# Optimization experiments

Measured on AMD Instinct MI355X. Metric: run time of the kernel, lower is better.

The kernel has to match this reference:

```python
import jax, jax.numpy as jnp
import numpy as np

B_SZ, SEQ, D_MODEL = 2, 4096, 2048
EXPAND, D_STATE, D_CONV = 2, 16, 4
D_INNER = EXPAND * D_MODEL          # 4096
DT_RANK = -(-D_MODEL // 16)         # 128


def setup_inputs() -> dict:
    key = jax.random.key(0)
    ks = jax.random.split(key, 9)
    s = 0.02
    hidden_states = jax.random.normal(ks[0], (B_SZ, SEQ, D_MODEL), jnp.float32)
    W_in = jax.random.normal(ks[1], (2 * D_INNER, D_MODEL), jnp.float32) * s
    conv_w = jax.random.normal(ks[2], (D_INNER, D_CONV), jnp.float32) * 0.2
    conv_b = jnp.zeros((D_INNER,), jnp.float32)
    W_x = jax.random.normal(ks[3], (DT_RANK + 2 * D_STATE, D_INNER), jnp.float32) * s
    W_dt = jax.random.normal(ks[4], (D_INNER, DT_RANK), jnp.float32) * (DT_RANK ** -0.5)
    # dt bias so softplus(dt) ~ [1e-3, 0.1] as in Mamba init
    u = jax.random.uniform(ks[5], (D_INNER,), jnp.float32)
    dt = jnp.exp(u * (np.log(0.1) - np.log(1e-3)) + np.log(1e-3))
    dt_bias = dt + jnp.log(-jnp.expm1(-dt))  # inverse softplus
    # S4D-real init: A = -[1..d_state] per channel (kept negative for stability)
    A = -jnp.tile(jnp.arange(1.0, D_STATE + 1.0, dtype=jnp.float32), (D_INNER, 1))
    D = jnp.ones((D_INNER,), jnp.float32)
    W_out = jax.random.normal(ks[6], (D_MODEL, D_INNER), jnp.float32) * s
    return {"hidden_states": hidden_states, "W_in": W_in, "conv_w": conv_w,
            "conv_b": conv_b, "W_x": W_x, "W_dt": W_dt, "dt_bias": dt_bias,
            "A": A, "D": D, "W_out": W_out}


def _mamba_fwd(hidden_states, W_in, conv_w, conv_b, W_x, W_dt, dt_bias, A, D, W_out):
    # in_proj -> (B, L, 2*d_inner); split into x and gate z
    xz = jnp.einsum('bld,ed->ble', hidden_states, W_in)
    x, z = jnp.split(xz, 2, axis=-1)                    # (B,L,d_inner) each
    # causal depthwise conv1d over L (kernel d_conv), then SiLU
    d_conv = conv_w.shape[1]
    xp = jnp.pad(x, ((0, 0), (d_conv - 1, 0), (0, 0)))
    L = x.shape[1]
    xc = conv_b
    acc = jnp.zeros_like(x)
    for k in range(d_conv):                             # small fixed loop (4 taps)
        acc = acc + xp[:, k:k + L, :] * conv_w[:, k]
    x = jax.nn.silu(acc + conv_b)
    # x_proj -> dt_rank + 2*d_state
    ssm = jnp.einsum('bld,ed->ble', x, W_x)
    dt_r, Bm, Cm = jnp.split(ssm, [DT_RANK, DT_RANK + D_STATE], axis=-1)
    delta = jax.nn.softplus(jnp.einsum('blr,dr->bld', dt_r, W_dt) + dt_bias)
    # selective scan: h_t = exp(delta_t*A) h_{t-1} + delta_t*B_t*u_t ; y_t = C_t.h_t
    def step(state, inp):
        d_t, u_t, B_t, C_t = inp                        # (B,Di),(B,Di),(B,N),(B,N)
        dA = jnp.exp(d_t[..., None] * A)                # (B,Di,N)
        state = state * dA + (d_t * u_t)[..., None] * B_t[:, None, :]
        y = jnp.einsum('bdn,bn->bd', state, C_t)
        return state, y
    init = jnp.zeros((x.shape[0], D_INNER, D_STATE), jnp.float32)
    xs = (jnp.swapaxes(delta, 0, 1), jnp.swapaxes(x, 0, 1),
          jnp.swapaxes(Bm, 0, 1), jnp.swapaxes(Cm, 0, 1))
    _, ys = jax.lax.scan(step, init, xs)
    y = jnp.swapaxes(ys, 0, 1) + x * D                  # D skip connection
    y = y * jax.nn.silu(z)                              # gate
    return jnp.einsum('bld,md->blm', y, W_out)


def reference(hidden_states, W_in, conv_w, conv_b, W_x, W_dt, dt_bias, A, D, W_out):
    return _mamba_fwd(hidden_states, W_in, conv_w, conv_b, W_x, W_dt,
                      dt_bias, A, D, W_out)
```

## Files before the change

### kernel.cpp

```cpp
#include <hip/hip_runtime.h>
#include <hip/hip_bf16.h>
#include <cstdint>
#include <cstddef>

typedef _Float16 f16x8 __attribute__((ext_vector_type(8)));
typedef _Float16 f16x4 __attribute__((ext_vector_type(4)));
typedef float    f32x4 __attribute__((ext_vector_type(4)));

#define AS1 __attribute__((address_space(1)))
#define AS3 __attribute__((address_space(3)))

static constexpr int B_SZ = 2, SEQ = 4096, D_MODEL = 2048;
static constexpr int D_INNER = 4096, D_STATE = 16, D_CONV = 4, DT_RANK = 128;
static constexpr int M_ROWS = B_SZ * SEQ;
static constexpr int SSM_W  = DT_RANK + 2 * D_STATE;

__global__ __launch_bounds__(256) void k_cvt_all(
    const float* __restrict__ s0, const float* __restrict__ s1,
    const float* __restrict__ s2, const float* __restrict__ s3,
    const float* __restrict__ s4,
    _Float16* __restrict__ d0, _Float16* __restrict__ d1,
    _Float16* __restrict__ d2, _Float16* __restrict__ d3,
    _Float16* __restrict__ d4) {
    const int i = blockIdx.x * 256 + threadIdx.x;
    const float* s; _Float16* d; int off;
    if (i < 4194304)      { s = s0; d = d0; off = i; }
    else if (i < 8388608) { s = s1; d = d1; off = i - 4194304; }
    else if (i < 8552448) { s = s2; d = d2; off = i - 8388608; }
    else if (i < 8683520) { s = s3; d = d3; off = i - 8552448; }
    else                  { s = s4; d = d4; off = i - 8683520; }
    f32x4 v = ((const f32x4*)s)[off];
    f16x4 h;
    h[0] = (_Float16)v[0]; h[1] = (_Float16)v[1];
    h[2] = (_Float16)v[2]; h[3] = (_Float16)v[3];
    ((f16x4*)d)[off] = h;
}

template <int EPI>
__global__ __launch_bounds__(512, 2) void k_gemm256p(
    const _Float16* __restrict__ A, const _Float16* __restrict__ Bm, int K, int nby,
    void* __restrict__ out0, void* __restrict__ out1, int ldc) {
    __shared__ _Float16 lA[2][256][64];
    __shared__ _Float16 lB[2][256][64];
    constexpr int LBUF  = 32768;
    constexpr int LBUFH = 16384;

    const int tid = threadIdx.x, l = tid & 63, w = tid >> 6;
    const int fr = l & 15, fq = l >> 4;
    const int wrA = (w >> 2) * 128;
    const int wcB = (w & 3) * 64;

    const int nwg = gridDim.x, qq = nwg >> 3;
    const int id = (blockIdx.x & 7) * qq + (blockIdx.x >> 3);
    const int by = id % nby, bx = id / nby;
    const int tileM = by * 256, tileN = bx * 256;

    const int rsub = l >> 3;
    const int gco  = ((l & 7) ^ rsub) << 3;
    const int swz0 = (fq ^ (fr & 7)) << 4;

    const char* cA = (const char*)lA;
    const char* cB = (const char*)lB;
    const int bA0 = (wrA + fr) * 128 + swz0;
    const int bA1 = bA0 ^ 64;
    const int bB0 = (wcB + fr) * 128 + swz0;
    const int bB1 = bB0 ^ 64;

    const _Float16* pA[4];
    const _Float16* pB[4];
    _Float16* dA[4];
    _Float16* dB[4];
#pragma unroll
    for (int u = 0; u < 4; ++u) {
        const int brow = (u >> 1) * 128 + (w * 2 + (u & 1)) * 8;
        pA[u] = A  + (size_t)(tileM + brow + rsub) * K + gco;
        pB[u] = Bm + (size_t)(tileN + brow + rsub) * K + gco;
        dA[u] = &lA[0][brow][0];
        dB[u] = &lB[0][brow][0];
    }

    const int NK = K >> 6;

    f32x4 acc[8][4];
#pragma unroll
    for (int m = 0; m < 8; m++)
#pragma unroll
        for (int n = 0; n < 4; n++) acc[m][n] = (f32x4)0.f;

#pragma unroll
    for (int t = 0; t < 2; ++t) {
#pragma unroll
        for (int u = 0; u < 4; ++u)
            __builtin_amdgcn_global_load_lds((const AS1 void*)(pA[u] + t * 64),
                (AS3 void*)(dA[u] + t * LBUFH), 16, 0, 0);
#pragma unroll
        for (int u = 0; u < 4; ++u)
            __builtin_amdgcn_global_load_lds((const AS1 void*)(pB[u] + t * 64),
                (AS3 void*)(dB[u] + t * LBUFH), 16, 0, 0);
    }
#pragma unroll
    for (int u = 0; u < 4; ++u) { pA[u] += 128; pB[u] += 128; }
    asm volatile("s_waitcnt vmcnt(8)" ::: "memory");
    __builtin_amdgcn_s_barrier();

    f16x8 af[4][2], bf0[2][2], bf1[2][2];

#define MFMA_QUAD(MO, NO, BF)                                                        \
    __builtin_amdgcn_s_setprio(1);                                                   \
    _Pragma("unroll") for (int m = 0; m < 4; ++m)                                    \
    _Pragma("unroll") for (int n = 0; n < 2; ++n)                                    \
    _Pragma("unroll") for (int kk = 0; kk < 2; ++kk)                                 \
        acc[(MO) + m][(NO) + n] = __builtin_amdgcn_mfma_f32_16x16x32_f16(            \
            af[m][kk], BF[n][kk], acc[(MO) + m][(NO) + n], 0, 0, 0);                 \
    __builtin_amdgcn_s_setprio(0);

#define KTILE(BUF, KOFF, PF, DOEND)                                                  \
          \
    _Pragma("unroll")                                                                \
    for (int m = 0; m < 4; ++m) {                                                    \
        af[m][0] = *(const f16x8*)(cA + (BUF) * LBUF + bA0 + m * 2048);              \
        af[m][1] = *(const f16x8*)(cA + (BUF) * LBUF + bA1 + m * 2048);              \
    }                                                                                \
    _Pragma("unroll")                                                                \
    for (int n = 0; n < 2; ++n) {                                                    \
        bf0[n][0] = *(const f16x8*)(cB + (BUF) * LBUF + bB0 + n * 2048);             \
        bf0[n][1] = *(const f16x8*)(cB + (BUF) * LBUF + bB1 + n * 2048);             \
    }                                                                                \
    _Pragma("unroll")                                                                \
    for (int n = 0; n < 2; ++n) {                                                    \
        bf1[n][0] = *(const f16x8*)(cB + (BUF) * LBUF + bB0 + (n + 2) * 2048);       \
        bf1[n][1] = *(const f16x8*)(cB + (BUF) * LBUF + bB1 + (n + 2) * 2048);       \
    }                                                                                \
    asm volatile("s_waitcnt lgkmcnt(4)" ::: "memory");     \
    __builtin_amdgcn_sched_barrier(0);                                               \
    MFMA_QUAD(0, 0, bf0)                                                             \
    asm volatile("s_waitcnt lgkmcnt(0)" ::: "memory");                 \
    __builtin_amdgcn_sched_barrier(0);                                               \
    MFMA_QUAD(0, 2, bf1)                                                             \
    __builtin_amdgcn_s_barrier();                \
    _Pragma("unroll")                                                                \
    for (int m = 0; m < 4; ++m) {                                                    \
        af[m][0] = *(const f16x8*)(cA + (BUF) * LBUF + bA0 + (m + 4) * 2048);        \
        af[m][1] = *(const f16x8*)(cA + (BUF) * LBUF + bA1 + (m + 4) * 2048);        \
    }                                                                                \
    if (PF) {                                                                        \
        _Pragma("unroll")                                                            \
        for (int u = 0; u < 4; ++u)                                                  \
            __builtin_amdgcn_global_load_lds((const AS1 void*)(pB[u] + (KOFF)),      \
                (AS3 void*)(dB[u] + (BUF) * LBUFH), 16, 0, 0);                       \
    }                                                                                \
    asm volatile("s_waitcnt lgkmcnt(0)" ::: "memory");               \
    __builtin_amdgcn_sched_barrier(0);                                               \
    MFMA_QUAD(4, 0, bf0)                                                             \
    __builtin_amdgcn_s_barrier();               \
    if (PF) {                                                                        \
        _Pragma("unroll")                                                            \
        for (int u = 0; u < 4; ++u)                                                  \
            __builtin_amdgcn_global_load_lds((const AS1 void*)(pA[u] + (KOFF)),      \
                (AS3 void*)(dA[u] + (BUF) * LBUFH), 16, 0, 0);                       \
    }                                                                                \
    MFMA_QUAD(4, 2, bf1)                                                             \
    if (DOEND) {                                                                     \
        if (PF) { asm volatile("s_waitcnt vmcnt(8)" ::: "memory"); }                 \
        else    { asm volatile("s_waitcnt vmcnt(0)" ::: "memory"); }                 \
        __builtin_amdgcn_s_barrier();                 \
    }

    for (int kt = 0; kt < NK; kt += 2) {
        const bool pf0 = (kt + 2 < NK);
        const bool pf1 = (kt + 3 < NK);
        KTILE(0, 0, pf0, true)
        KTILE(1, 64, pf1, pf0)
#pragma unroll
        for (int u = 0; u < 4; ++u) { pA[u] += 128; pB[u] += 128; }
    }
#undef KTILE
#undef MFMA_QUAD

#pragma unroll
    for (int m = 0; m < 8; ++m) {
#pragma unroll
        for (int n = 0; n < 4; ++n) {
            const int r0 = tileM + wrA + m * 16 + fq * 4;
            const int c  = tileN + wcB + n * 16 + fr;
#pragma unroll
            for (int q = 0; q < 4; ++q) {
                const float  v  = acc[m][n][q];
                const size_t mm = (size_t)(r0 + q);
                if (EPI == 0) {
                    if (c < D_INNER)
                        ((_Float16*)out0)[mm * D_INNER + c] = (_Float16)v;
                    else
                        ((_Float16*)out1)[mm * D_INNER + (c - D_INNER)] = (_Float16)v;
                } else {
                    ((float*)out0)[mm * ldc + c] = v;
                }
            }
        }
    }
}

template <int BM, int BN, int EPI>
__global__ __launch_bounds__(256) void k_gemm_nt(
    const _Float16* __restrict__ A, const _Float16* __restrict__ Bm, int K,
    int lda, int ldb, void* __restrict__ out0, void* __restrict__ out1,
    const float* __restrict__ bias, int ldc) {
    __shared__ _Float16 a_lds[BM][32];
    __shared__ _Float16 b_lds[BN][32];
    constexpr int MR = BM / 32;
    constexpr int NR = BN / 32;
    const int tid  = threadIdx.x;
    const int lane = tid & 63;
    const int wid  = tid >> 6;
    const int wr = wid >> 1, wc = wid & 1;
    const int tileM = blockIdx.y * BM;
    const int tileN = blockIdx.x * BN;

    f32x4 acc[MR][NR];
    for (int i = 0; i < MR; i++)
        for (int j = 0; j < NR; j++) acc[i][j] = (f32x4)0.f;

    constexpr int IS_A = BM / 16;
    constexpr int IS_B = BN / 16;
    const int srow = lane >> 2;
    const int skof = (lane & 3) * 8;
    const int fr = lane & 15, fq = lane >> 4;

    for (int kk = 0; kk < K; kk += 32) {
        if (kk) __syncthreads();
        for (int is = wid; is < IS_A + IS_B; is += 4) {
            const bool isA = is < IS_A;
            const int  li  = isA ? is : is - IS_A;
            const int  row = li * 16 + srow;
            const _Float16* g =
                isA ? (A  + (size_t)(tileM + row) * lda + kk + skof)
                    : (Bm + (size_t)(tileN + row) * ldb + kk + skof);
            char* lp = ((char*)(isA ? &a_lds[0][0] : &b_lds[0][0])) + (size_t)li * 1024;
            __builtin_amdgcn_global_load_lds((const AS1 void*)g, (AS3 void*)lp, 16, 0, 0);
        }
        __syncthreads();

        f16x8 af[MR], bf[NR];
#pragma unroll
        for (int i = 0; i < MR; i++)
            af[i] = *(const f16x8*)&a_lds[wr * (BM / 2) + i * 16 + fr][fq * 8];
#pragma unroll
        for (int j = 0; j < NR; j++)
            bf[j] = *(const f16x8*)&b_lds[wc * (BN / 2) + j * 16 + fr][fq * 8];
#pragma unroll
        for (int i = 0; i < MR; i++)
#pragma unroll
            for (int j = 0; j < NR; j++)
                acc[i][j] = __builtin_amdgcn_mfma_f32_16x16x32_f16(af[i], bf[j], acc[i][j], 0, 0, 0);
    }

#pragma unroll
    for (int i = 0; i < MR; i++) {
#pragma unroll
        for (int j = 0; j < NR; j++) {
            const int r0 = tileM + wr * (BM / 2) + i * 16 + fq * 4;
            const int c  = tileN + wc * (BN / 2) + j * 16 + fr;
#pragma unroll
            for (int q = 0; q < 4; q++) {
                const float  v = acc[i][j][q];
                const size_t m = (size_t)(r0 + q);
                if (EPI == 1) {
                    ((float*)out0)[m * ldc + c] = v;
                } else if (EPI == 2) {
                    float x  = v + bias[c];
                    float sp = (x > 20.f) ? x : log1pf(__expf(x));
                    ((_Float16*)out0)[m * ldc + c] = (_Float16)sp;
                } else {
                    ((float*)out0)[m * ldc + c] = v;
                    if (c < DT_RANK)
                        ((_Float16*)out1)[m * DT_RANK + c] = (_Float16)v;
                }
            }
        }
    }
}

__global__ __launch_bounds__(256) void k_conv_silu(const _Float16* __restrict__ x,
                                                   const float* __restrict__ w,
                                                   const float* __restrict__ bias,
                                                   _Float16* __restrict__ out) {
    const int idx = blockIdx.x * 256 + threadIdx.x;
    const int d4 = idx & (D_INNER / 4 - 1);
    const int t  = (idx >> 10) & (SEQ - 1);
    const int b  = idx >> 22;
    const int d  = d4 * 4;
    const size_t rowbase = (size_t)b * SEQ * D_INNER;

    f32x4 wv[4];
#pragma unroll
    for (int i = 0; i < 4; i++) wv[i] = ((const f32x4*)w)[d + i];

    float acc[4];
#pragma unroll
    for (int i = 0; i < 4; i++) acc[i] = bias[d + i];
#pragma unroll
    for (int k = 0; k < D_CONV; k++) {
        int ti = t - (D_CONV - 1) + k;
        if (ti < 0) continue;
        f16x4 xv = *(const f16x4*)&x[rowbase + (size_t)ti * D_INNER + d];
#pragma unroll
        for (int i = 0; i < 4; i++) acc[i] += (float)xv[i] * wv[i][k];
    }
    f16x4 o;
#pragma unroll
    for (int i = 0; i < 4; i++) {
        float v = acc[i];
        o[i] = (_Float16)(v / (1.f + __expf(-v)));
    }
    *(f16x4*)&out[rowbase + (size_t)t * D_INNER + d] = o;
}

template <int CH, typename ST>
__global__ __launch_bounds__(256) void k_scan_p1(const _Float16* __restrict__ delta_h,
                                                 const _Float16* __restrict__ xc,
                                                 const float* __restrict__ ssm,
                                                 const float* __restrict__ Aptr,
                                                 ST* __restrict__ Sbuf,
                                                 ST* __restrict__ Pbuf) {
    constexpr int NCH = SEQ / CH;
    constexpr float L2E = 1.44269504088896f;
    const int bid   = blockIdx.x;
    const int dg    = bid & 15;
    const int chunk = (bid >> 4) % NCH;
    const int b     = bid / (16 * NCH);
    const int d     = dg * 256 + threadIdx.x;

    __shared__ float bsh[CH][D_STATE];
    const size_t rb = (size_t)b * SEQ + (size_t)chunk * CH;
    for (int i = threadIdx.x; i < CH * D_STATE; i += 256) {
        int t = i >> 4, n = i & 15;
        bsh[t][n] = ssm[(rb + t) * SSM_W + DT_RANK + n];
    }
    __syncthreads();

    float a2[D_STATE];
#pragma unroll
    for (int n = 0; n < D_STATE; n++) a2[n] = Aptr[(size_t)d * D_STATE + n] * L2E;
    float st[D_STATE];
#pragma unroll
    for (int n = 0; n < D_STATE; n++) st[n] = 0.f;
    float dtsum = 0.f;

    for (int t = 0; t < CH; ++t) {
        const size_t idx = (rb + t) * D_INNER + d;
        const float dt = (float)delta_h[idx];
        const float u  = (float)xc[idx];
        const float du = dt * u;
        dtsum += dt;
#pragma unroll
        for (int n = 0; n < D_STATE; n++) {
            float p = exp2f(dt * a2[n]);
            st[n] = st[n] * p + du * bsh[t][n];
        }
    }
    const size_t ob = ((size_t)(b * NCH + chunk) * D_STATE) * D_INNER + d;
#pragma unroll
    for (int n = 0; n < D_STATE; n++) {
        Sbuf[ob + (size_t)n * D_INNER] = (ST)st[n];
        Pbuf[ob + (size_t)n * D_INNER] = (ST)exp2f(dtsum * a2[n]);
    }
}

template <int NCH, typename ST>
__global__ __launch_bounds__(256) void k_scan_p2(ST* __restrict__ Sbuf,
                                                 const ST* __restrict__ Pbuf) {
    const int id = blockIdx.x * 256 + threadIdx.x;
    const int d = id & (D_INNER - 1);
    const int n = (id >> 12) & 15;
    const int b = id >> 16;
    float h = 0.f;
    for (int c = 0; c < NCH; ++c) {
        const size_t off = ((size_t)((b * NCH + c) * D_STATE + n)) * D_INNER + d;
        const float Pv = (float)Pbuf[off];
        const float Sv = (float)Sbuf[off];
        Sbuf[off] = (ST)h;
        h = Pv * h + Sv;
    }
}

template <int CH, typename ST>
__global__ __launch_bounds__(256) void k_scan_p3(const _Float16* __restrict__ delta_h,
                                                 const _Float16* __restrict__ xc,
                                                 const float* __restrict__ ssm,
                                                 const _Float16* __restrict__ z,
                                                 const float* __restrict__ Aptr,
                                                 const float* __restrict__ Dptr,
                                                 const ST* __restrict__ Sbuf,
                                                 _Float16* __restrict__ y_out) {
    constexpr int NCH = SEQ / CH;
    constexpr float L2E = 1.44269504088896f;
    const int bid   = blockIdx.x;
    const int dg    = bid & 15;
    const int chunk = (bid >> 4) % NCH;
    const int b     = bid / (16 * NCH);
    const int d     = dg * 256 + threadIdx.x;

    __shared__ float bsh[CH][2 * D_STATE];
    const size_t rb = (size_t)b * SEQ + (size_t)chunk * CH;
    for (int i = threadIdx.x; i < CH * 2 * D_STATE; i += 256) {
        int t = i >> 5, j = i & 31;
        bsh[t][j] = ssm[(rb + t) * SSM_W + DT_RANK + j];
    }
    __syncthreads();

    float a2[D_STATE];
#pragma unroll
    for (int n = 0; n < D_STATE; n++) a2[n] = Aptr[(size_t)d * D_STATE + n] * L2E;
    const float Dd = Dptr[d];

    const size_t ob = ((size_t)(b * NCH + chunk) * D_STATE) * D_INNER + d;
    float st[D_STATE];
#pragma unroll
    for (int n = 0; n < D_STATE; n++) st[n] = (float)Sbuf[ob + (size_t)n * D_INNER];

    for (int t = 0; t < CH; ++t) {
        const size_t idx = (rb + t) * D_INNER + d;
        const float dt = (float)delta_h[idx];
        const float u  = (float)xc[idx];
        const float du = dt * u;
        float y = 0.f;
#pragma unroll
        for (int n = 0; n < D_STATE; n++) {
            float p = exp2f(dt * a2[n]);
            st[n] = st[n] * p + du * bsh[t][n];
            y += st[n] * bsh[t][D_STATE + n];
        }
        const float zv = (float)z[idx];
        const float g  = zv / (1.f + __expf(-zv));
        y_out[idx] = (_Float16)((y + u * Dd) * g);
    }
}

__global__ __launch_bounds__(256) void k_scan(const _Float16* __restrict__ delta_h,
                                              const _Float16* __restrict__ xc,
                                              const float* __restrict__ ssm,
                                              const _Float16* __restrict__ z,
                                              const float* __restrict__ Aptr,
                                              const float* __restrict__ Dptr,
                                              _Float16* __restrict__ y_out) {
    const int b = blockIdx.x >> 4;
    const int d = (blockIdx.x & 15) * 256 + threadIdx.x;
    constexpr float L2E = 1.44269504088896f;
    float a2[D_STATE];
#pragma unroll
    for (int n = 0; n < D_STATE; n++) a2[n] = Aptr[(size_t)d * D_STATE + n] * L2E;
    const float Dd = Dptr[d];
    float st[D_STATE];
#pragma unroll
    for (int n = 0; n < D_STATE; n++) st[n] = 0.f;
    __shared__ float bc[128][32];
    const size_t rb = (size_t)b * SEQ;
    for (int tc = 0; tc < SEQ; tc += 128) {
        __syncthreads();
        for (int i = threadIdx.x; i < 128 * 32; i += 256) {
            int tl = i >> 5, j = i & 31;
            bc[tl][j] = ssm[(rb + tc + tl) * SSM_W + DT_RANK + j];
        }
        __syncthreads();
        for (int tl = 0; tl < 128; ++tl) {
            const size_t idx = (rb + tc + tl) * D_INNER + d;
            const float dt = (float)delta_h[idx];
            const float u  = (float)xc[idx];
            const float du = dt * u;
            float y = 0.f;
#pragma unroll
            for (int n = 0; n < D_STATE; n++) {
                float dA = exp2f(dt * a2[n]);
                st[n] = st[n] * dA + du * bc[tl][n];
                y += st[n] * bc[tl][D_STATE + n];
            }
            const float zv = (float)z[idx];
            const float g  = zv / (1.f + __expf(-zv));
            y_out[idx] = (_Float16)((y + u * Dd) * g);
        }
    }
}

template <int CH, typename ST>
static void launch_chunked_scan(const _Float16* delta_h, const _Float16* xc,
                                const float* ssm, const _Float16* z,
                                const float* Aptr, const float* Dptr,
                                ST* S, ST* P, _Float16* y, hipStream_t stream) {
    constexpr int NCH = SEQ / CH;
    k_scan_p1<CH, ST><<<B_SZ * NCH * 16, 256, 0, stream>>>(delta_h, xc, ssm, Aptr, S, P);
    k_scan_p2<NCH, ST><<<(B_SZ * 16 * D_INNER) / 256, 256, 0, stream>>>(S, P);
    k_scan_p3<CH, ST><<<B_SZ * NCH * 16, 256, 0, stream>>>(delta_h, xc, ssm, z, Aptr, Dptr, S, y);
}

extern "C" void kernel_launch(void* const* d_in, const int* in_sizes, int n_in,
                              void* d_out, int out_size, void* d_ws, size_t ws_size,
                              hipStream_t stream) {
    const float* hs    = (const float*)d_in[0];
    const float* W_in  = (const float*)d_in[1];
    const float* convw = (const float*)d_in[2];
    const float* convb = (const float*)d_in[3];
    const float* W_x   = (const float*)d_in[4];
    const float* W_dt  = (const float*)d_in[5];
    const float* dtb   = (const float*)d_in[6];
    const float* Aptr  = (const float*)d_in[7];
    const float* Dptr  = (const float*)d_in[8];
    const float* W_out = (const float*)d_in[9];

    char* ws = (char*)d_ws;
    _Float16* hs_h    = (_Float16*)(ws + 0);
    _Float16* Win_h   = (_Float16*)(ws + 33554432);
    _Float16* y_h     = (_Float16*)(ws + 0);
    _Float16* xraw    = (_Float16*)(ws + 67108864);
    _Float16* delta_h = (_Float16*)(ws + 67108864);
    _Float16* xc      = (_Float16*)(ws + 134217728);
    float*    ssm     = (float*)   (ws + 201326592);
    _Float16* dtr     = (_Float16*)(ws + 206569472);
    _Float16* Wx_h    = (_Float16*)(ws + 208666624);
    _Float16* Wdt_h   = (_Float16*)(ws + 209977344);
    _Float16* Wout_h  = (_Float16*)(ws + 211025920);
    _Float16* z_h     = (_Float16*)d_out;
    const size_t spbase = 227803136ull;

    k_cvt_all<<<42112, 256, 0, stream>>>(hs, W_in, W_x, W_dt, W_out,
                                         hs_h, Win_h, Wx_h, Wdt_h, Wout_h);

    k_gemm256p<0><<<(M_ROWS / 256) * (2 * D_INNER / 256), 512, 0, stream>>>(
        hs_h, Win_h, D_MODEL, M_ROWS / 256, xraw, z_h, 0);

    k_conv_silu<<<(B_SZ * SEQ * (D_INNER / 4)) / 256, 256, 0, stream>>>(xraw, convw, convb, xc);

    k_gemm_nt<128, 32, 3><<<dim3(SSM_W / 32, M_ROWS / 128), 256, 0, stream>>>(
        xc, Wx_h, D_INNER, D_INNER, D_INNER, ssm, dtr, nullptr, SSM_W);

    k_gemm_nt<128, 128, 2><<<dim3(D_INNER / 128, M_ROWS / 128), 256, 0, stream>>>(
        dtr, Wdt_h, DT_RANK, DT_RANK, DT_RANK, delta_h, nullptr, dtb, D_INNER);

    {
        const size_t e64  = (size_t)B_SZ * (SEQ / 64)  * D_STATE * D_INNER;
        const size_t e128 = (size_t)B_SZ * (SEQ / 128) * D_STATE * D_INNER;
        if (ws_size >= spbase + 2 * e64 * sizeof(float)) {
            float* S = (float*)(ws + spbase);
            float* P = S + e64;
            launch_chunked_scan<64, float>(delta_h, xc, ssm, z_h, Aptr, Dptr, S, P, y_h, stream);
        } else if (ws_size >= spbase + 2 * e128 * sizeof(float)) {
            float* S = (float*)(ws + spbase);
            float* P = S + e128;
            launch_chunked_scan<128, float>(delta_h, xc, ssm, z_h, Aptr, Dptr, S, P, y_h, stream);
        } else if (ws_size >= spbase + 2 * e128 * sizeof(_Float16)) {
            _Float16* S = (_Float16*)(ws + spbase);
            _Float16* P = S + e128;
            launch_chunked_scan<128, _Float16>(delta_h, xc, ssm, z_h, Aptr, Dptr, S, P, y_h, stream);
        } else {
            k_scan<<<B_SZ * (D_INNER / 256), 256, 0, stream>>>(delta_h, xc, ssm, z_h, Aptr, Dptr, y_h);
        }
    }

    k_gemm256p<1><<<(M_ROWS / 256) * (D_MODEL / 256), 512, 0, stream>>>(
        y_h, Wout_h, D_INNER, M_ROWS / 256, d_out, nullptr, D_MODEL);
}
```

Baseline: 1.119 ms.

## Fuse dt projection and softplus into chunked scan kernels; restructure big GEMM pipeline

Removes the separate dt_proj GEMM that wrote the full delta tensor to global memory. Both scan passes now recompute delta for their chunk with MFMA from dtr and W_dt, apply bias and softplus, and keep it in LDS. This avoids writing and twice re-reading a large fp16 delta tensor, at the cost of doing the small rank-128 GEMM twice and using more LDS per block. The 256x256 GEMM main loop is also reorganised into k-halves: A fragments for the next tile are preloaded, and A and B are both staged right after a single barrier, replacing the interleaved quadrant schedule.

Result: slower. 2.530 ms (+126.2%).

```diff
diff --git a/kernel.cpp b/kernel.cpp
--- a/kernel.cpp
+++ b/kernel.cpp
@@ -42,8 +42,7 @@
     void* __restrict__ out0, void* __restrict__ out1, int ldc) {
     __shared__ _Float16 lA[2][256][64];
     __shared__ _Float16 lB[2][256][64];
-    constexpr int LBUF  = 32768;
-    constexpr int LBUFH = 16384;
+    constexpr int LBUF = 32768;
 
     const int tid = threadIdx.x, l = tid & 63, w = tid >> 6;
     const int fr = l & 15, fq = l >> 4;
@@ -66,18 +65,9 @@
     const int bB0 = (wcB + fr) * 128 + swz0;
     const int bB1 = bB0 ^ 64;
 
-    const _Float16* pA[4];
-    const _Float16* pB[4];
-    _Float16* dA[4];
-    _Float16* dB[4];
-#pragma unroll
-    for (int u = 0; u < 4; ++u) {
-        const int brow = (u >> 1) * 128 + (w * 2 + (u & 1)) * 8;
-        pA[u] = A  + (size_t)(tileM + brow + rsub) * K + gco;
-        pB[u] = Bm + (size_t)(tileN + brow + rsub) * K + gco;
-        dA[u] = &lA[0][brow][0];
-        dB[u] = &lB[0][brow][0];
-    }
+    const _Float16* Abase = A  + (size_t)tileM * K;
+    const _Float16* Bbase = Bm + (size_t)tileN * K;
+    const int laneOff = rsub * K + gco;
 
     const int NK = K >> 6;
 
@@ -87,95 +77,82 @@
 #pragma unroll
         for (int n = 0; n < 4; n++) acc[m][n] = (f32x4)0.f;
 
-#pragma unroll
-    for (int t = 0; t < 2; ++t) {
-#pragma unroll
-        for (int u = 0; u < 4; ++u)
-            __builtin_amdgcn_global_load_lds((const AS1 void*)(pA[u] + t * 64),
-                (AS3 void*)(dA[u] + t * LBUFH), 16, 0, 0);
-#pragma unroll
-        for (int u = 0; u < 4; ++u)
-            __builtin_amdgcn_global_load_lds((const AS1 void*)(pB[u] + t * 64),
-                (AS3 void*)(dB[u] + t * LBUFH), 16, 0, 0);
-    }
-#pragma unroll
-    for (int u = 0; u < 4; ++u) { pA[u] += 128; pB[u] += 128; }
+#define STAGE_AB(KT2)                                                                 \
+    {                                                                                 \
+        const size_t ko = (size_t)(KT2) * 64;                                         \
+        const int bsel = (KT2) & 1;                                                   \
+        _Pragma("unroll")                                                             \
+        for (int u = 0; u < 4; ++u) {                                                 \
+            const int brow = (u >> 1) * 128 + (w * 2 + (u & 1)) * 8;                  \
+            __builtin_amdgcn_global_load_lds(                                         \
+                (const AS1 void*)(Abase + (size_t)brow * K + ko + laneOff),           \
+                (AS3 void*)&lA[bsel][brow][0], 16, 0, 0);                             \
+        }                                                                             \
+        _Pragma("unroll")                                                             \
+        for (int u = 0; u < 4; ++u) {                                                 \
+            const int brow = (u >> 1) * 128 + (w * 2 + (u & 1)) * 8;                  \
+            __builtin_amdgcn_global_load_lds(                                         \
+                (const AS1 void*)(Bbase + (size_t)brow * K + ko + laneOff),           \
+                (AS3 void*)&lB[bsel][brow][0], 16, 0, 0);                             \
+        }                                                                             \
+    }
+
+    STAGE_AB(0)
+    STAGE_AB(1)
     asm volatile("s_waitcnt vmcnt(8)" ::: "memory");
     __builtin_amdgcn_s_barrier();
 
-    f16x8 af[4][2], bf0[2][2], bf1[2][2];
-
-#define MFMA_QUAD(MO, NO, BF)                                                        \
-    __builtin_amdgcn_s_setprio(1);                                                   \
-    _Pragma("unroll") for (int m = 0; m < 4; ++m)                                    \
-    _Pragma("unroll") for (int n = 0; n < 2; ++n)                                    \
-    _Pragma("unroll") for (int kk = 0; kk < 2; ++kk)                                 \
-        acc[(MO) + m][(NO) + n] = __builtin_amdgcn_mfma_f32_16x16x32_f16(            \
-            af[m][kk], BF[n][kk], acc[(MO) + m][(NO) + n], 0, 0, 0);                 \
+    f16x8 afk0[8], afk1[8], bfk0[4], bfk1[4];
+#pragma unroll
+    for (int m = 0; m < 8; ++m)
+        afk0[m] = *(const f16x8*)(cA + bA0 + m * 2048);
+
+#define MFMA_HALF(AF, BF)                                                             \
+    __builtin_amdgcn_s_setprio(1);                                                    \
+    _Pragma("unroll") for (int m = 0; m < 8; ++m)                                     \
+    _Pragma("unroll") for (int n = 0; n < 4; ++n)                                     \
+        acc[m][n] = __builtin_amdgcn_mfma_f32_16x16x32_f16(                           \
+            AF[m], BF[n], acc[m][n], 0, 0, 0);                                        \
     __builtin_amdgcn_s_setprio(0);
 
-#define KTILE(BUF, KOFF, PF, DOEND)                                                  \
-          \
-    _Pragma("unroll")                                                                \
-    for (int m = 0; m < 4; ++m) {                                                    \
-        af[m][0] = *(const f16x8*)(cA + (BUF) * LBUF + bA0 + m * 2048);              \
-        af[m][1] = *(const f16x8*)(cA + (BUF) * LBUF + bA1 + m * 2048);              \
-    }                                                                                \
-    _Pragma("unroll")                                                                \
-    for (int n = 0; n < 2; ++n) {                                                    \
-        bf0[n][0] = *(const f16x8*)(cB + (BUF) * LBUF + bB0 + n * 2048);             \
-        bf0[n][1] = *(const f16x8*)(cB + (BUF) * LBUF + bB1 + n * 2048);             \
-    }                                                                                \
-    _Pragma("unroll")                                                                \
-    for (int n = 0; n < 2; ++n) {                                                    \
-        bf1[n][0] = *(const f16x8*)(cB + (BUF) * LBUF + bB0 + (n + 2) * 2048);       \
-        bf1[n][1] = *(const f16x8*)(cB + (BUF) * LBUF + bB1 + (n + 2) * 2048);       \
-    }                                                                                \
-    asm volatile("s_waitcnt lgkmcnt(4)" ::: "memory");     \
-    __builtin_amdgcn_sched_barrier(0);                                               \
-    MFMA_QUAD(0, 0, bf0)                                                             \
-    asm volatile("s_waitcnt lgkmcnt(0)" ::: "memory");                 \
-    __builtin_amdgcn_sched_barrier(0);                                               \
-    MFMA_QUAD(0, 2, bf1)                                                             \
-    __builtin_amdgcn_s_barrier();                \
-    _Pragma("unroll")                                                                \
-    for (int m = 0; m < 4; ++m) {                                                    \
-        af[m][0] = *(const f16x8*)(cA + (BUF) * LBUF + bA0 + (m + 4) * 2048);        \
-        af[m][1] = *(const f16x8*)(cA + (BUF) * LBUF + bA1 + (m + 4) * 2048);        \
-    }                                                                                \
-    if (PF) {                                                                        \
-        _Pragma("unroll")                                                            \
-        for (int u = 0; u < 4; ++u)                                                  \
-            __builtin_amdgcn_global_load_lds((const AS1 void*)(pB[u] + (KOFF)),      \
-                (AS3 void*)(dB[u] + (BUF) * LBUFH), 16, 0, 0);                       \
-    }                                                                                \
-    asm volatile("s_waitcnt lgkmcnt(0)" ::: "memory");               \
-    __builtin_amdgcn_sched_barrier(0);                                               \
-    MFMA_QUAD(4, 0, bf0)                                                             \
-    __builtin_amdgcn_s_barrier();               \
-    if (PF) {                                                                        \
-        _Pragma("unroll")                                                            \
-        for (int u = 0; u < 4; ++u)                                                  \
-            __builtin_amdgcn_global_load_lds((const AS1 void*)(pA[u] + (KOFF)),      \
-                (AS3 void*)(dA[u] + (BUF) * LBUFH), 16, 0, 0);                       \
-    }                                                                                \
-    MFMA_QUAD(4, 2, bf1)                                                             \
-    if (DOEND) {                                                                     \
-        if (PF) { asm volatile("s_waitcnt vmcnt(8)" ::: "memory"); }                 \
-        else    { asm volatile("s_waitcnt vmcnt(0)" ::: "memory"); }                 \
-        __builtin_amdgcn_s_barrier();                 \
-    }
+#define KTILE(BUF, NBUF, PF, HN, KT2)                                                 \
+                                      \
+    _Pragma("unroll")                                                                 \
+    for (int n = 0; n < 4; ++n)                                                       \
+        bfk0[n] = *(const f16x8*)(cB + (BUF) * LBUF + bB0 + n * 2048);                \
+    _Pragma("unroll")                                                                 \
+    for (int m = 0; m < 8; ++m)                                                       \
+        afk1[m] = *(const f16x8*)(cA + (BUF) * LBUF + bA1 + m * 2048);                \
+    _Pragma("unroll")                                                                 \
+    for (int n = 0; n < 4; ++n)                                                       \
+        bfk1[n] = *(const f16x8*)(cB + (BUF) * LBUF + bB1 + n * 2048);                \
+    asm volatile("s_waitcnt lgkmcnt(12)" ::: "memory");          \
+    __builtin_amdgcn_sched_barrier(0);                                                \
+    MFMA_HALF(afk0, bfk0)                                                             \
+    asm volatile("s_waitcnt lgkmcnt(0)" ::: "memory");     \
+    __builtin_amdgcn_sched_barrier(0);                                                \
+    __builtin_amdgcn_s_barrier();                              \
+    if (PF) STAGE_AB(KT2)                                                             \
+    if (HN) {                                                                         \
+        if (PF) { asm volatile("s_waitcnt vmcnt(8)" ::: "memory"); }                  \
+        else    { asm volatile("s_waitcnt vmcnt(0)" ::: "memory"); }                  \
+        __builtin_amdgcn_s_barrier();                          \
+        _Pragma("unroll")                                                             \
+        for (int m = 0; m < 8; ++m)                                                   \
+            afk0[m] = *(const f16x8*)(cA + (NBUF) * LBUF + bA0 + m * 2048);           \
+    }                                                                                 \
+    __builtin_amdgcn_sched_barrier(0);                                                \
+    MFMA_HALF(afk1, bfk1)
 
     for (int kt = 0; kt < NK; kt += 2) {
         const bool pf0 = (kt + 2 < NK);
         const bool pf1 = (kt + 3 < NK);
-        KTILE(0, 0, pf0, true)
-        KTILE(1, 64, pf1, pf0)
-#pragma unroll
-        for (int u = 0; u < 4; ++u) { pA[u] += 128; pB[u] += 128; }
+        KTILE(0, 1, pf0, true, kt + 2)
+        KTILE(1, 0, pf1, pf0, kt + 3)
     }
 #undef KTILE
-#undef MFMA_QUAD
+#undef MFMA_HALF
+#undef STAGE_AB
 
 #pragma unroll
     for (int m = 0; m < 8; ++m) {
@@ -316,28 +293,71 @@
 }
 
 template <int CH, typename ST>
-__global__ __launch_bounds__(256) void k_scan_p1(const _Float16* __restrict__ delta_h,
+__global__ __launch_bounds__(256) void k_scan_p1(const _Float16* __restrict__ dtr,
+                                                 const _Float16* __restrict__ Wdt,
+                                                 const float* __restrict__ dtb,
                                                  const _Float16* __restrict__ xc,
                                                  const float* __restrict__ ssm,
                                                  const float* __restrict__ Aptr,
                                                  ST* __restrict__ Sbuf,
                                                  ST* __restrict__ Pbuf) {
     constexpr int NCH = SEQ / CH;
+    constexpr int MR  = CH / 16;
     constexpr float L2E = 1.44269504088896f;
     const int bid   = blockIdx.x;
     const int dg    = bid & 15;
     const int chunk = (bid >> 4) % NCH;
     const int b     = bid / (16 * NCH);
-    const int d     = dg * 256 + threadIdx.x;
-
-    __shared__ float bsh[CH][D_STATE];
+    const int tid   = threadIdx.x;
+    const int lane  = tid & 63, wid = tid >> 6;
+    const int fr = lane & 15, fq = lane >> 4;
     const size_t rb = (size_t)b * SEQ + (size_t)chunk * CH;
-    for (int i = threadIdx.x; i < CH * D_STATE; i += 256) {
+
+    __shared__ float    bsh[CH][D_STATE];
+    __shared__ _Float16 dsh[CH][256];
+
+    {
+        f32x4 acc[MR][4];
+#pragma unroll
+        for (int i = 0; i < MR; ++i)
+#pragma unroll
+            for (int j = 0; j < 4; ++j) acc[i][j] = (f32x4)0.f;
+        const int nbase = wid * 64;
+        for (int kk = 0; kk < DT_RANK; kk += 32) {
+            f16x8 af[MR], bf[4];
+#pragma unroll
+            for (int i = 0; i < MR; ++i)
+                af[i] = *(const f16x8*)&dtr[(rb + i * 16 + fr) * DT_RANK + kk + fq * 8];
+#pragma unroll
+            for (int j = 0; j < 4; ++j)
+                bf[j] = *(const f16x8*)&Wdt[(size_t)(dg * 256 + nbase + j * 16 + fr) * DT_RANK + kk + fq * 8];
+#pragma unroll
+            for (int i = 0; i < MR; ++i)
+#pragma unroll
+                for (int j = 0; j < 4; ++j)
+                    acc[i][j] = __builtin_amdgcn_mfma_f32_16x16x32_f16(af[i], bf[j], acc[i][j], 0, 0, 0);
+        }
+#pragma unroll
+        for (int j = 0; j < 4; ++j) {
+            const int c  = nbase + j * 16 + fr;
+            const float bv = dtb[dg * 256 + c];
+#pragma unroll
+            for (int i = 0; i < MR; ++i)
+#pragma unroll
+                for (int q = 0; q < 4; ++q) {
+                    float x  = acc[i][j][q] + bv;
+                    float sp = (x > 20.f) ? x : log1pf(__expf(x));
+                    dsh[i * 16 + fq * 4 + q][c] = (_Float16)sp;
+                }
+        }
+    }
+    for (int i = tid; i < CH * D_STATE; i += 256) {
         int t = i >> 4, n = i & 15;
         bsh[t][n] = ssm[(rb + t) * SSM_W + DT_RANK + n];
     }
     __syncthreads();
 
+    const int d = dg * 256 + tid;
     float a2[D_STATE];
 #pragma unroll
     for (int n = 0; n < D_STATE; n++) a2[n] = Aptr[(size_t)d * D_STATE + n] * L2E;
@@ -347,9 +367,8 @@
     float dtsum = 0.f;
 
     for (int t = 0; t < CH; ++t) {
-        const size_t idx = (rb + t) * D_INNER + d;
-        const float dt = (float)delta_h[idx];
-        const float u  = (float)xc[idx];
+        const float dt = (float)dsh[t][tid];
+        const float u  = (float)xc[(rb + t) * D_INNER + d];
         const float du = dt * u;
         dtsum += dt;
 #pragma unroll
@@ -384,7 +403,9 @@
 }
 
 template <int CH, typename ST>
-__global__ __launch_bounds__(256) void k_scan_p3(const _Float16* __restrict__ delta_h,
+__global__ __launch_bounds__(256) void k_scan_p3(const _Float16* __restrict__ dtr,
+                                                 const _Float16* __restrict__ Wdt,
+                                                 const float* __restrict__ dtb,
                                                  const _Float16* __restrict__ xc,
                                                  const float* __restrict__ ssm,
                                                  const _Float16* __restrict__ z,
@@ -393,21 +414,62 @@
                                                  const ST* __restrict__ Sbuf,
                                                  _Float16* __restrict__ y_out) {
     constexpr int NCH = SEQ / CH;
+    constexpr int MR  = CH / 16;
     constexpr float L2E = 1.44269504088896f;
     const int bid   = blockIdx.x;
     const int dg    = bid & 15;
     const int chunk = (bid >> 4) % NCH;
     const int b     = bid / (16 * NCH);
-    const int d     = dg * 256 + threadIdx.x;
-
-    __shared__ float bsh[CH][2 * D_STATE];
+    const int tid   = threadIdx.x;
+    const int lane  = tid & 63, wid = tid >> 6;
+    const int fr = lane & 15, fq = lane >> 4;
     const size_t rb = (size_t)b * SEQ + (size_t)chunk * CH;
-    for (int i = threadIdx.x; i < CH * 2 * D_STATE; i += 256) {
+
+    __shared__ float    bsh[CH][2 * D_STATE];
+    __shared__ _Float16 dsh[CH][256];
+
+    {
+        f32x4 acc[MR][4];
+#pragma unroll
+        for (int i = 0; i < MR; ++i)
+#pragma unroll
+            for (int j = 0; j < 4; ++j) acc[i][j] = (f32x4)0.f;
+        const int nbase = wid * 64;
+        for (int kk = 0; kk < DT_RANK; kk += 32) {
+            f16x8 af[MR], bf[4];
+#pragma unroll
+            for (int i = 0; i < MR; ++i)
+                af[i] = *(const f16x8*)&dtr[(rb + i * 16 + fr) * DT_RANK + kk + fq * 8];
+#pragma unroll
+            for (int j = 0; j < 4; ++j)
+                bf[j] = *(const f16x8*)&Wdt[(size_t)(dg * 256 + nbase + j * 16 + fr) * DT_RANK + kk + fq * 8];
+#pragma unroll
+            for (int i = 0; i < MR; ++i)
+#pragma unroll
+                for (int j = 0; j < 4; ++j)
+                    acc[i][j] = __builtin_amdgcn_mfma_f32_16x16x32_f16(af[i], bf[j], acc[i][j], 0, 0, 0);
+        }
+#pragma unroll
+        for (int j = 0; j < 4; ++j) {
+            const int c  = nbase + j * 16 + fr;
+            const float bv = dtb[dg * 256 + c];
+#pragma unroll
+            for (int i = 0; i < MR; ++i)
+#pragma unroll
+                for (int q = 0; q < 4; ++q) {
+                    float x  = acc[i][j][q] + bv;
+                    float sp = (x > 20.f) ? x : log1pf(__expf(x));
+                    dsh[i * 16 + fq * 4 + q][c] = (_Float16)sp;
+                }
+        }
+    }
+    for (int i = tid; i < CH * 2 * D_STATE; i += 256) {
         int t = i >> 5, j = i & 31;
         bsh[t][j] = ssm[(rb + t) * SSM_W + DT_RANK + j];
     }
     __syncthreads();
 
+    const int d = dg * 256 + tid;
     float a2[D_STATE];
 #pragma unroll
     for (int n = 0; n < D_STATE; n++) a2[n] = Aptr[(size_t)d * D_STATE + n] * L2E;
@@ -420,7 +482,7 @@
 
     for (int t = 0; t < CH; ++t) {
         const size_t idx = (rb + t) * D_INNER + d;
-        const float dt = (float)delta_h[idx];
+        const float dt = (float)dsh[t][tid];
         const float u  = (float)xc[idx];
         const float du = dt * u;
         float y = 0.f;
@@ -482,14 +544,15 @@
 }
 
 template <int CH, typename ST>
-static void launch_chunked_scan(const _Float16* delta_h, const _Float16* xc,
+static void launch_chunked_scan(const _Float16* dtr, const _Float16* Wdt,
+                                const float* dtb, const _Float16* xc,
                                 const float* ssm, const _Float16* z,
                                 const float* Aptr, const float* Dptr,
                                 ST* S, ST* P, _Float16* y, hipStream_t stream) {
     constexpr int NCH = SEQ / CH;
-    k_scan_p1<CH, ST><<<B_SZ * NCH * 16, 256, 0, stream>>>(delta_h, xc, ssm, Aptr, S, P);
+    k_scan_p1<CH, ST><<<B_SZ * NCH * 16, 256, 0, stream>>>(dtr, Wdt, dtb, xc, ssm, Aptr, S, P);
     k_scan_p2<NCH, ST><<<(B_SZ * 16 * D_INNER) / 256, 256, 0, stream>>>(S, P);
-    k_scan_p3<CH, ST><<<B_SZ * NCH * 16, 256, 0, stream>>>(delta_h, xc, ssm, z, Aptr, Dptr, S, y);
+    k_scan_p3<CH, ST><<<B_SZ * NCH * 16, 256, 0, stream>>>(dtr, Wdt, dtb, xc, ssm, z, Aptr, Dptr, S, y);
 }
 
 extern "C" void kernel_launch(void* const* d_in, const int* in_sizes, int n_in,
@@ -532,25 +595,24 @@
     k_gemm_nt<128, 32, 3><<<dim3(SSM_W / 32, M_ROWS / 128), 256, 0, stream>>>(
         xc, Wx_h, D_INNER, D_INNER, D_INNER, ssm, dtr, nullptr, SSM_W);
 
-    k_gemm_nt<128, 128, 2><<<dim3(D_INNER / 128, M_ROWS / 128), 256, 0, stream>>>(
-        dtr, Wdt_h, DT_RANK, DT_RANK, DT_RANK, delta_h, nullptr, dtb, D_INNER);
-
     {
         const size_t e64  = (size_t)B_SZ * (SEQ / 64)  * D_STATE * D_INNER;
         const size_t e128 = (size_t)B_SZ * (SEQ / 128) * D_STATE * D_INNER;
         if (ws_size >= spbase + 2 * e64 * sizeof(float)) {
             float* S = (float*)(ws + spbase);
             float* P = S + e64;
-            launch_chunked_scan<64, float>(delta_h, xc, ssm, z_h, Aptr, Dptr, S, P, y_h, stream);
+            launch_chunked_scan<64, float>(dtr, Wdt_h, dtb, xc, ssm, z_h, Aptr, Dptr, S, P, y_h, stream);
         } else if (ws_size >= spbase + 2 * e128 * sizeof(float)) {
             float* S = (float*)(ws + spbase);
             float* P = S + e128;
-            launch_chunked_scan<128, float>(delta_h, xc, ssm, z_h, Aptr, Dptr, S, P, y_h, stream);
+            launch_chunked_scan<128, float>(dtr, Wdt_h, dtb, xc, ssm, z_h, Aptr, Dptr, S, P, y_h, stream);
         } else if (ws_size >= spbase + 2 * e128 * sizeof(_Float16)) {
             _Float16* S = (_Float16*)(ws + spbase);
             _Float16* P = S + e128;
-            launch_chunked_scan<128, _Float16>(delta_h, xc, ssm, z_h, Aptr, Dptr, S, P, y_h, stream);
+            launch_chunked_scan<128, _Float16>(dtr, Wdt_h, dtb, xc, ssm, z_h, Aptr, Dptr, S, P, y_h, stream);
         } else {
+            k_gemm_nt<128, 128, 2><<<dim3(D_INNER / 128, M_ROWS / 128), 256, 0, stream>>>(
+                dtr, Wdt_h, DT_RANK, DT_RANK, DT_RANK, delta_h, nullptr, dtb, D_INNER);
             k_scan<<<B_SZ * (D_INNER / 256), 256, 0, stream>>>(delta_h, xc, ssm, z_h, Aptr, Dptr, y_h);
         }
     }
```

## Split-K the x_proj GEMM with a reduction kernel and unroll scan time loops

Applied to the files above, without the earlier changes.

The narrow x_proj GEMM (N=160, K=4096) is split along K into 8 slices with smaller M tiles, raising block count and occupancy. Partial sums go to a scratch buffer and a new reduction kernel sums them and writes both ssm and the fp16 dt_rank copy. The chunked scan passes also unroll their time loop by 4 to batch the delta/x/z loads ahead of the recurrence. The trade is extra global traffic for the partial buffer plus one more kernel launch.

After: 1.099 ms. About the same (-1.7%).

```diff
diff --git a/kernel.cpp b/kernel.cpp
--- a/kernel.cpp
+++ b/kernel.cpp
@@ -14,6 +14,7 @@
 static constexpr int D_INNER = 4096, D_STATE = 16, D_CONV = 4, DT_RANK = 128;
 static constexpr int M_ROWS = B_SZ * SEQ;
 static constexpr int SSM_W  = DT_RANK + 2 * D_STATE;
+static constexpr int KSPLIT = 8, KSLICE = 512;
 
 __global__ __launch_bounds__(256) void k_cvt_all(
     const float* __restrict__ s0, const float* __restrict__ s1,
@@ -215,6 +216,7 @@
     const int wr = wid >> 1, wc = wid & 1;
     const int tileM = blockIdx.y * BM;
     const int tileN = blockIdx.x * BN;
+    const int kz = (EPI == 4) ? blockIdx.z * KSLICE : 0;
 
     f32x4 acc[MR][NR];
     for (int i = 0; i < MR; i++)
@@ -233,8 +235,8 @@
             const int  li  = isA ? is : is - IS_A;
             const int  row = li * 16 + srow;
             const _Float16* g =
-                isA ? (A  + (size_t)(tileM + row) * lda + kk + skof)
-                    : (Bm + (size_t)(tileN + row) * ldb + kk + skof);
+                isA ? (A  + (size_t)(tileM + row) * lda + kz + kk + skof)
+                    : (Bm + (size_t)(tileN + row) * ldb + kz + kk + skof);
             char* lp = ((char*)(isA ? &a_lds[0][0] : &b_lds[0][0])) + (size_t)li * 1024;
             __builtin_amdgcn_global_load_lds((const AS1 void*)g, (AS3 void*)lp, 16, 0, 0);
         }
@@ -270,14 +272,30 @@
                     float x  = v + bias[c];
                     float sp = (x > 20.f) ? x : log1pf(__expf(x));
                     ((_Float16*)out0)[m * ldc + c] = (_Float16)sp;
-                } else {
+                } else if (EPI == 3) {
                     ((float*)out0)[m * ldc + c] = v;
                     if (c < DT_RANK)
                         ((_Float16*)out1)[m * DT_RANK + c] = (_Float16)v;
+                } else {
+                    ((float*)out0)[(size_t)blockIdx.z * M_ROWS * SSM_W + m * ldc + c] = v;
                 }
             }
         }
     }
+}
+
+__global__ __launch_bounds__(256) void k_xred(const float* __restrict__ pbuf,
+                                              float* __restrict__ ssm,
+                                              _Float16* __restrict__ dtr) {
+    const int i = blockIdx.x * 256 + threadIdx.x;
+    const int m = i / SSM_W;
+    const int c = i - m * SSM_W;
+    float s = 0.f;
+#pragma unroll
+    for (int z = 0; z < KSPLIT; ++z)
+        s += pbuf[(size_t)z * M_ROWS * SSM_W + i];
+    ssm[i] = s;
+    if (c < DT_RANK) dtr[(size_t)m * DT_RANK + c] = (_Float16)s;
 }
 
 __global__ __launch_bounds__(256) void k_conv_silu(const _Float16* __restrict__ x,
@@ -346,16 +364,23 @@
     for (int n = 0; n < D_STATE; n++) st[n] = 0.f;
     float dtsum = 0.f;
 
-    for (int t = 0; t < CH; ++t) {
-        const size_t idx = (rb + t) * D_INNER + d;
-        const float dt = (float)delta_h[idx];
-        const float u  = (float)xc[idx];
-        const float du = dt * u;
-        dtsum += dt;
-#pragma unroll
-        for (int n = 0; n < D_STATE; n++) {
-            float p = exp2f(dt * a2[n]);
-            st[n] = st[n] * p + du * bsh[t][n];
+    for (int t = 0; t < CH; t += 4) {
+        const size_t i0 = (rb + t) * D_INNER + d;
+        float dtv[4], uv[4];
+#pragma unroll
+        for (int j = 0; j < 4; ++j) {
+            dtv[j] = (float)delta_h[i0 + (size_t)j * D_INNER];
+            uv[j]  = (float)xc[i0 + (size_t)j * D_INNER];
+        }
+#pragma unroll
+        for (int j = 0; j < 4; ++j) {
+            const float du = dtv[j] * uv[j];
+            dtsum += dtv[j];
+#pragma unroll
+            for (int n = 0; n < D_STATE; n++) {
+                float p = exp2f(dtv[j] * a2[n]);
+                st[n] = st[n] * p + du * bsh[t + j][n];
+            }
         }
     }
     const size_t ob = ((size_t)(b * NCH + chunk) * D_STATE) * D_INNER + d;
@@ -418,21 +443,28 @@
 #pragma unroll
     for (int n = 0; n < D_STATE; n++) st[n] = (float)Sbuf[ob + (size_t)n * D_INNER];
 
-    for (int t = 0; t < CH; ++t) {
-        const size_t idx = (rb + t) * D_INNER + d;
-        const float dt = (float)delta_h[idx];
-        const float u  = (float)xc[idx];
-        const float du = dt * u;
-        float y = 0.f;
-#pragma unroll
-        for (int n = 0; n < D_STATE; n++) {
-            float p = exp2f(dt * a2[n]);
-            st[n] = st[n] * p + du * bsh[t][n];
-            y += st[n] * bsh[t][D_STATE + n];
-        }
-        const float zv = (float)z[idx];
-        const float g  = zv / (1.f + __expf(-zv));
-        y_out[idx] = (_Float16)((y + u * Dd) * g);
+    for (int t = 0; t < CH; t += 4) {
+        const size_t i0 = (rb + t) * D_INNER + d;
+        float dtv[4], uv[4], zv[4];
+#pragma unroll
+        for (int j = 0; j < 4; ++j) {
+            dtv[j] = (float)delta_h[i0 + (size_t)j * D_INNER];
+            uv[j]  = (float)xc[i0 + (size_t)j * D_INNER];
+            zv[j]  = (float)z[i0 + (size_t)j * D_INNER];
+        }
+#pragma unroll
+        for (int j = 0; j < 4; ++j) {
+            const float du = dtv[j] * uv[j];
+            float y = 0.f;
+#pragma unroll
+            for (int n = 0; n < D_STATE; n++) {
+                float p = exp2f(dtv[j] * a2[n]);
+                st[n] = st[n] * p + du * bsh[t + j][n];
+                y += st[n] * bsh[t + j][D_STATE + n];
+            }
+            const float g = zv[j] / (1.f + __expf(-zv[j]));
+            y_out[i0 + (size_t)j * D_INNER] = (_Float16)((y + uv[j] * Dd) * g);
+        }
     }
 }
 
@@ -511,6 +543,7 @@
     _Float16* Win_h   = (_Float16*)(ws + 33554432);
     _Float16* y_h     = (_Float16*)(ws + 0);
     _Float16* xraw    = (_Float16*)(ws + 67108864);
+    float*    pbuf    = (float*)   (ws + 67108864);
     _Float16* delta_h = (_Float16*)(ws + 67108864);
     _Float16* xc      = (_Float16*)(ws + 134217728);
     float*    ssm     = (float*)   (ws + 201326592);
@@ -529,8 +562,9 @@
 
     k_conv_silu<<<(B_SZ * SEQ * (D_INNER / 4)) / 256, 256, 0, stream>>>(xraw, convw, convb, xc);
 
-    k_gemm_nt<128, 32, 3><<<dim3(SSM_W / 32, M_ROWS / 128), 256, 0, stream>>>(
-        xc, Wx_h, D_INNER, D_INNER, D_INNER, ssm, dtr, nullptr, SSM_W);
+    k_gemm_nt<64, 32, 4><<<dim3(SSM_W / 32, M_ROWS / 64, KSPLIT), 256, 0, stream>>>(
+        xc, Wx_h, KSLICE, D_INNER, D_INNER, pbuf, nullptr, nullptr, SSM_W);
+    k_xred<<<(M_ROWS * SSM_W) / 256, 256, 0, stream>>>(pbuf, ssm, dtr);
 
     k_gemm_nt<128, 128, 2><<<dim3(D_INNER / 128, M_ROWS / 128), 256, 0, stream>>>(
         dtr, Wdt_h, DT_RANK, DT_RANK, DT_RANK, delta_h, nullptr, dtb, D_INNER);
```
